# Performance work log

Hardware: AMD Instinct MI355X
Metric: run time of the kernel (lower is better)

Reference implementation:

```python
import jax, jax.numpy as jnp
import numpy as np

N_NODES = 100000
N_EDGES = 1600000
D = 64


def setup_inputs() -> dict:
    key = jax.random.key(0)
    k0, k1, k2, k3 = jax.random.split(key, 4)
    x = jax.random.normal(k0, (N_NODES, D), dtype=jnp.float32)
    edge_index = jax.random.randint(k1, (2, N_EDGES), 0, N_NODES, dtype=jnp.int64)
    W1 = jax.random.normal(k2, (D, D), dtype=jnp.float32) * 0.1
    b1 = jnp.zeros((D,), dtype=jnp.float32)
    W2 = jax.random.normal(k3, (D, D), dtype=jnp.float32) * 0.1
    b2 = jnp.zeros((D,), dtype=jnp.float32)
    return {"x": x, "edge_index": edge_index, "W1": W1, "b1": b1, "W2": W2, "b2": b2}


def _gcn_layer(x, edge_index, W, b):
    n = x.shape[0]
    h = x @ W  # [N, Dout] -- transform before aggregation (small GEMM)
    loop = jnp.arange(n, dtype=edge_index.dtype)
    src = jnp.concatenate([edge_index[0], loop])
    dst = jnp.concatenate([edge_index[1], loop])
    deg = jax.ops.segment_sum(jnp.ones_like(dst, dtype=h.dtype), dst, num_segments=n)
    dinv = jax.lax.rsqrt(deg)  # deg >= 1 thanks to self loops
    norm = dinv[src] * dinv[dst]  # [E+N]
    msg = h[src] * norm[:, None]  # gather: [E+N, Dout]
    agg = jax.ops.segment_sum(msg, dst, num_segments=n)  # scatter-add
    return agg + b


def reference(x, edge_index, W1, b1, W2, b2):
    # dropout p = 0.0 -> identity
    h = jax.nn.relu(_gcn_layer(x, edge_index, W1, b1))
    h = jax.nn.relu(_gcn_layer(h, edge_index, W2, b2))
    return h
```

## Files before the change

### kernel.cpp

```cpp
#include <hip/hip_runtime.h>
#include <hip/hip_bf16.h>

#define D 64
#define NB_HIST 256
#define MAXBK 512

typedef float vfloat4 __attribute__((ext_vector_type(4)));
typedef short short8 __attribute__((ext_vector_type(8)));
typedef float f32x4 __attribute__((ext_vector_type(4)));

__device__ __forceinline__ unsigned short f2bf(float f) {
    union { float f; unsigned u; } v; v.f = f;
    unsigned r = (v.u + 0x7FFF + ((v.u >> 16) & 1)) >> 16;
    return (unsigned short)r;
}
__device__ __forceinline__ unsigned short bftrunc(float f) {
    union { float f; unsigned u; } v; v.f = f;
    return (unsigned short)(v.u >> 16);
}
__device__ __forceinline__ float bffrom(unsigned short h) {
    union { unsigned u; float f; } v; v.u = ((unsigned)h) << 16; return v.f;
}
__device__ __forceinline__ float bflo(unsigned u) {
    union { unsigned u; float f; } v; v.u = u << 16; return v.f;
}
__device__ __forceinline__ float bfhi(unsigned u) {
    union { unsigned u; float f; } v; v.u = u & 0xFFFF0000u; return v.f;
}

__global__ __launch_bounds__(256) void passA_hist_wfrag(
    const int* __restrict__ dst, int* __restrict__ blockCounts, int E, int per, int NBK,
    const float* __restrict__ W1, const float* __restrict__ W2,
    unsigned short* __restrict__ WfH1, unsigned short* __restrict__ WfL1,
    unsigned short* __restrict__ WfH2, unsigned short* __restrict__ WfL2)
{
    int tid = threadIdx.x;

    if ((int)blockIdx.x < NB_HIST) {
        __shared__ int hist[MAXBK];
        for (int i = tid; i < NBK; i += 256) hist[i] = 0;
        __syncthreads();
        int lo = blockIdx.x * per, hi = min(E, lo + per);
        for (int i = lo + tid * 4; i < hi; i += 1024) {
            if (i + 3 < hi) {
                int4 d4 = *(const int4*)(dst + i);
                atomicAdd(&hist[d4.x >> 8], 1);
                atomicAdd(&hist[d4.y >> 8], 1);
                atomicAdd(&hist[d4.z >> 8], 1);
                atomicAdd(&hist[d4.w >> 8], 1);
            } else {
                for (int k = i; k < hi; ++k) atomicAdd(&hist[dst[k] >> 8], 1);
            }
        }
        __syncthreads();
        for (int i = tid; i < NBK; i += 256)
            blockCounts[(size_t)blockIdx.x * NBK + i] = hist[i];
        return;
    }

    int b = (int)blockIdx.x - NB_HIST;
    const float* Wsrc = (b >> 1) ? W2 : W1;
    unsigned short* fh = (b >> 1) ? WfH2 : WfH1;
    unsigned short* fl = (b >> 1) ? WfL2 : WfL1;
    int combo = (b & 1) * 4 + (tid >> 6);
    int lane = tid & 63;
    int s = combo >> 2, c = combo & 3, g = lane >> 4, rl = lane & 15;
#pragma unroll
    for (int j = 0; j < 8; ++j) {
        float v = Wsrc[(32 * s + 8 * g + j) * D + 16 * c + rl];
        unsigned short h = bftrunc(v);
        fh[combo * 512 + lane * 8 + j] = h;
        fl[combo * 512 + lane * 8 + j] = f2bf(v - bffrom(h));
    }
}

__global__ __launch_bounds__(256) void scan_cols(
    const int* __restrict__ blockCounts, int* __restrict__ partial,
    int* __restrict__ totals, int NBK)
{
    int wave = threadIdx.x >> 6, lane = threadIdx.x & 63;
    int k = blockIdx.x * 4 + wave;
    if (k >= NBK) return;
    int carry = 0;
    for (int base = 0; base < NB_HIST; base += 64) {
        int b = base + lane;
        int v = blockCounts[(size_t)b * NBK + k];
        int inc = v;
        for (int d = 1; d < 64; d <<= 1) {
            int t = __shfl_up(inc, d, 64);
            if (lane >= d) inc += t;
        }
        partial[(size_t)k * NB_HIST + b] = inc - v + carry;
        carry += __shfl(inc, 63, 64);
    }
    if (lane == 0) totals[k] = carry;
}

__global__ void scan_buckets(const int* __restrict__ totals, int* __restrict__ bofs, int NBK) {
    int lane = threadIdx.x;
    int carry = 0;
    for (int base = 0; base < NBK; base += 64) {
        int i = base + lane;
        int v = (i < NBK) ? totals[i] : 0;
        int inc = v;
        for (int d = 1; d < 64; d <<= 1) {
            int t = __shfl_up(inc, d, 64);
            if (lane >= d) inc += t;
        }
        if (i < NBK) bofs[i] = inc - v + carry;
        carry += __shfl(inc, 63, 64);
    }
}

__global__ __launch_bounds__(256) void passB(
    const int* __restrict__ src, const int* __restrict__ dst,
    const int* __restrict__ bofs, const int* __restrict__ partial,
    int* __restrict__ bucketed, int E, int per, int NBK)
{
    __shared__ int cur[MAXBK];
    int tid = threadIdx.x, b = blockIdx.x;
    for (int i = tid; i < NBK; i += 256)
        cur[i] = bofs[i] + partial[(size_t)i * NB_HIST + b];
    __syncthreads();
    int lo = b * per, hi = min(E, lo + per);
    for (int i = lo + tid * 4; i < hi; i += 1024) {
        if (i + 3 < hi) {
            int4 d4 = *(const int4*)(dst + i);
            int4 s4 = *(const int4*)(src + i);
            int p0 = atomicAdd(&cur[d4.x >> 8], 1);
            int p1 = atomicAdd(&cur[d4.y >> 8], 1);
            int p2 = atomicAdd(&cur[d4.z >> 8], 1);
            int p3 = atomicAdd(&cur[d4.w >> 8], 1);
            bucketed[p0] = (s4.x << 8) | (d4.x & 255);
            bucketed[p1] = (s4.y << 8) | (d4.y & 255);
            bucketed[p2] = (s4.z << 8) | (d4.z & 255);
            bucketed[p3] = (s4.w << 8) | (d4.w & 255);
        } else {
            for (int k = i; k < hi; ++k) {
                int d = dst[k], s = src[k];
                int pos = atomicAdd(&cur[d >> 8], 1);
                bucketed[pos] = (s << 8) | (d & 255);
            }
        }
    }
}

__global__ __launch_bounds__(256) void build_csr(
    const int* __restrict__ bucketed, const int* __restrict__ bofs,
    const int* __restrict__ totals, int* __restrict__ deg, float* __restrict__ dinv,
    int* __restrict__ ofs, int* __restrict__ csr, int N)
{
    __shared__ int h[256];
    __shared__ int scn[256];
    int tid = threadIdx.x, k = blockIdx.x;
    int e0 = bofs[k], e1 = e0 + totals[k];
    int node = k * 256 + tid;

    h[tid] = 0;
    __syncthreads();
    for (int i = e0 + tid; i < e1; i += 256)
        atomicAdd(&h[bucketed[i] & 255], 1);
    __syncthreads();

    int mydeg = h[tid];
    scn[tid] = mydeg;
    __syncthreads();
    for (int d2 = 1; d2 < 256; d2 <<= 1) {
        int t = (tid >= d2) ? scn[tid - d2] : 0;
        __syncthreads();
        scn[tid] += t;
        __syncthreads();
    }
    int myofs = scn[tid] - mydeg;

    if (node < N) {
        deg[node]  = mydeg;
        dinv[node] = rsqrtf((float)(mydeg + 1));
        ofs[node]  = e0 + myofs;
    }

    h[tid] = myofs;
    __syncthreads();
    for (int i = e0 + tid; i < e1; i += 256) {
        int v = bucketed[i];
        int pos = atomicAdd(&h[v & 255], 1);
        csr[e0 + pos] = v >> 8;
    }
}

__global__ __launch_bounds__(256) void gemm1_mfma(
    const float* __restrict__ X,
    const unsigned short* __restrict__ WfH, const unsigned short* __restrict__ WfL,
    const float* __restrict__ dinv, unsigned short* __restrict__ hn, int N)
{
    int t = threadIdx.x, wave = t >> 6, lane = t & 63;
    int rowBase = (int)blockIdx.x * 64 + wave * 16;
    if (rowBase >= N) return;
    int g = lane >> 4, rl = lane & 15;

    short8 BH[2][4], BL[2][4];
#pragma unroll
    for (int s = 0; s < 2; ++s)
#pragma unroll
        for (int c = 0; c < 4; ++c) {
            BH[s][c] = *(const short8*)(WfH + ((s * 4 + c) * 64 + lane) * 8);
            BL[s][c] = *(const short8*)(WfL + ((s * 4 + c) * 64 + lane) * 8);
        }

    int arow = rowBase + rl; if (arow >= N) arow = N - 1;
    const float* xr = X + (size_t)arow * D;

    f32x4 acc[4];
#pragma unroll
    for (int c = 0; c < 4; ++c) acc[c] = (f32x4){0.f, 0.f, 0.f, 0.f};

#pragma unroll
    for (int s = 0; s < 2; ++s) {
        vfloat4 x0 = *(const vfloat4*)(xr + 32 * s + 8 * g);
        vfloat4 x1 = *(const vfloat4*)(xr + 32 * s + 8 * g + 4);
        short8 ah, al;
#pragma unroll
        for (int j = 0; j < 4; ++j) {
            unsigned short h0 = bftrunc(x0[j]);
            ah[j] = (short)h0; al[j] = (short)f2bf(x0[j] - bffrom(h0));
            unsigned short h1 = bftrunc(x1[j]);
            ah[j + 4] = (short)h1; al[j + 4] = (short)f2bf(x1[j] - bffrom(h1));
        }
#pragma unroll
        for (int c = 0; c < 4; ++c)
            acc[c] = __builtin_amdgcn_mfma_f32_16x16x32_bf16(ah, BH[s][c], acc[c], 0, 0, 0);
#pragma unroll
        for (int c = 0; c < 4; ++c)
            acc[c] = __builtin_amdgcn_mfma_f32_16x16x32_bf16(ah, BL[s][c], acc[c], 0, 0, 0);
#pragma unroll
        for (int c = 0; c < 4; ++c)
            acc[c] = __builtin_amdgcn_mfma_f32_16x16x32_bf16(al, BH[s][c], acc[c], 0, 0, 0);
    }

#pragma unroll
    for (int r = 0; r < 4; ++r) {
        int row = rowBase + g * 4 + r;
        if (row < N) {
            float dv = dinv[row];
            unsigned short* hr = hn + (size_t)row * D + rl;
#pragma unroll
            for (int c = 0; c < 4; ++c) hr[c * 16] = f2bf(acc[c][r] * dv);
        }
    }
}

__global__ __launch_bounds__(256) void agg1_gemm2(
    const int* __restrict__ ofs, const int* __restrict__ deg,
    const int* __restrict__ csr, const unsigned short* __restrict__ hnA,
    const float* __restrict__ dinv, const float* __restrict__ bias,
    const unsigned short* __restrict__ WfH, const unsigned short* __restrict__ WfL,
    unsigned short* __restrict__ hnB, int N)
{
    __shared__ unsigned short sH[32 * 72];
    int tid  = threadIdx.x;
    int lane = tid & 63, wave = tid >> 6;
    int grp  = lane >> 3, sub = lane & 7;
    int rowInBlk = wave * 8 + grp;
    int nodeBase = (int)blockIdx.x * 32;
    int node = nodeBase + rowInBlk;
    bool live = (node < N);

    const int4* hrow = (const int4*)hnA;
    float2 a0 = {0.f, 0.f}, a1 = {0.f, 0.f}, a2 = {0.f, 0.f}, a3 = {0.f, 0.f};

    int s0 = 0, cnt = 0;
    if (live) {
        s0  = ofs[node];
        cnt = deg[node];
        int4 h = hrow[(size_t)node * 8 + sub];
        a0.x += bflo(h.x); a0.y += bfhi(h.x);
        a1.x += bflo(h.y); a1.y += bfhi(h.y);
        a2.x += bflo(h.z); a2.y += bfhi(h.z);
        a3.x += bflo(h.w); a3.y += bfhi(h.w);
    }

    const int* cp = csr + s0;
    int j = 0;
    for (; j + 3 < cnt; j += 4) {
        int sA = cp[j], sB = cp[j + 1], sC = cp[j + 2], sD = cp[j + 3];
        int4 hA = hrow[(size_t)sA * 8 + sub];
        int4 hB = hrow[(size_t)sB * 8 + sub];
        int4 hC = hrow[(size_t)sC * 8 + sub];
        int4 hD = hrow[(size_t)sD * 8 + sub];
        a0.x += bflo(hA.x); a0.y += bfhi(hA.x);
        a1.x += bflo(hA.y); a1.y += bfhi(hA.y);
        a2.x += bflo(hA.z); a2.y += bfhi(hA.z);
        a3.x += bflo(hA.w); a3.y += bfhi(hA.w);
        a0.x += bflo(hB.x); a0.y += bfhi(hB.x);
        a1.x += bflo(hB.y); a1.y += bfhi(hB.y);
        a2.x += bflo(hB.z); a2.y += bfhi(hB.z);
        a3.x += bflo(hB.w); a3.y += bfhi(hB.w);
        a0.x += bflo(hC.x); a0.y += bfhi(hC.x);
        a1.x += bflo(hC.y); a1.y += bfhi(hC.y);
        a2.x += bflo(hC.z); a2.y += bfhi(hC.z);
        a3.x += bflo(hC.w); a3.y += bfhi(hC.w);
        a0.x += bflo(hD.x); a0.y += bfhi(hD.x);
        a1.x += bflo(hD.y); a1.y += bfhi(hD.y);
        a2.x += bflo(hD.z); a2.y += bfhi(hD.z);
        a3.x += bflo(hD.w); a3.y += bfhi(hD.w);
    }
    for (; j < cnt; ++j) {
        int sA = cp[j];
        int4 hA = hrow[(size_t)sA * 8 + sub];
        a0.x += bflo(hA.x); a0.y += bfhi(hA.x);
        a1.x += bflo(hA.y); a1.y += bfhi(hA.y);
        a2.x += bflo(hA.z); a2.y += bfhi(hA.z);
        a3.x += bflo(hA.w); a3.y += bfhi(hA.w);
    }

    {
        float dw = live ? dinv[node] : 0.f;
        float4 b0 = ((const float4*)bias)[sub * 2];
        float4 b1 = ((const float4*)bias)[sub * 2 + 1];
        float o0 = fmaxf(a0.x * dw + b0.x, 0.f);
        float o1 = fmaxf(a0.y * dw + b0.y, 0.f);
        float o2 = fmaxf(a1.x * dw + b0.z, 0.f);
        float o3 = fmaxf(a1.y * dw + b0.w, 0.f);
        float o4 = fmaxf(a2.x * dw + b1.x, 0.f);
        float o5 = fmaxf(a2.y * dw + b1.y, 0.f);
        float o6 = fmaxf(a3.x * dw + b1.z, 0.f);
        float o7 = fmaxf(a3.y * dw + b1.w, 0.f);
        unsigned r0 = (unsigned)f2bf(o0) | ((unsigned)f2bf(o1) << 16);
        unsigned r1 = (unsigned)f2bf(o2) | ((unsigned)f2bf(o3) << 16);
        unsigned r2 = (unsigned)f2bf(o4) | ((unsigned)f2bf(o5) << 16);
        unsigned r3 = (unsigned)f2bf(o6) | ((unsigned)f2bf(o7) << 16);
        *(int4*)&sH[rowInBlk * 72 + sub * 8] = make_int4((int)r0, (int)r1, (int)r2, (int)r3);
    }
    __syncthreads();

    if (wave < 2) {
        int g = lane >> 4, rl = lane & 15;
        f32x4 acc[4];
#pragma unroll
        for (int c = 0; c < 4; ++c) acc[c] = (f32x4){0.f, 0.f, 0.f, 0.f};

#pragma unroll
        for (int s = 0; s < 2; ++s) {
            short8 a = *(const short8*)&sH[(wave * 16 + rl) * 72 + 32 * s + 8 * g];
            short8 BH[4], BL[4];
#pragma unroll
            for (int c = 0; c < 4; ++c) {
                BH[c] = *(const short8*)(WfH + ((s * 4 + c) * 64 + lane) * 8);
                BL[c] = *(const short8*)(WfL + ((s * 4 + c) * 64 + lane) * 8);
            }
#pragma unroll
            for (int c = 0; c < 4; ++c)
                acc[c] = __builtin_amdgcn_mfma_f32_16x16x32_bf16(a, BH[c], acc[c], 0, 0, 0);
#pragma unroll
            for (int c = 0; c < 4; ++c)
                acc[c] = __builtin_amdgcn_mfma_f32_16x16x32_bf16(a, BL[c], acc[c], 0, 0, 0);
        }

#pragma unroll
        for (int r = 0; r < 4; ++r) {
            int row = nodeBase + wave * 16 + g * 4 + r;
            if (row < N) {
                float dv = dinv[row];
                unsigned short* hw = hnB + (size_t)row * D + rl;
#pragma unroll
                for (int c = 0; c < 4; ++c) hw[c * 16] = f2bf(acc[c][r] * dv);
            }
        }
    }
}

template <bool BF16OUT>
__global__ __launch_bounds__(256) void aggregate_relu(
    const int* __restrict__ ofs, const int* __restrict__ deg,
    const int* __restrict__ csr, const unsigned short* __restrict__ hn,
    const float* __restrict__ dinv, const float* __restrict__ bias,
    void* __restrict__ outv, int N)
{
    int t    = blockIdx.x * 256 + threadIdx.x;
    int lane = threadIdx.x & 63;
    int grp  = lane >> 3, sub = lane & 7;
    int node = (t >> 6) * 8 + grp;
    bool live = (node < N);

    const int4* hrow = (const int4*)hn;
    float2 a0 = {0.f, 0.f}, a1 = {0.f, 0.f}, a2 = {0.f, 0.f}, a3 = {0.f, 0.f};

    int s0 = 0, cnt = 0;
    if (live) {
        s0  = ofs[node];
        cnt = deg[node];
        int4 h = hrow[(size_t)node * 8 + sub];
        a0.x += bflo(h.x); a0.y += bfhi(h.x);
        a1.x += bflo(h.y); a1.y += bfhi(h.y);
        a2.x += bflo(h.z); a2.y += bfhi(h.z);
        a3.x += bflo(h.w); a3.y += bfhi(h.w);
    }

    const int* cp = csr + s0;
    int j = 0;
    for (; j + 3 < cnt; j += 4) {
        int sA = cp[j], sB = cp[j + 1], sC = cp[j + 2], sD = cp[j + 3];
        int4 hA = hrow[(size_t)sA * 8 + sub];
        int4 hB = hrow[(size_t)sB * 8 + sub];
        int4 hC = hrow[(size_t)sC * 8 + sub];
        int4 hD = hrow[(size_t)sD * 8 + sub];
        a0.x += bflo(hA.x); a0.y += bfhi(hA.x);
        a1.x += bflo(hA.y); a1.y += bfhi(hA.y);
        a2.x += bflo(hA.z); a2.y += bfhi(hA.z);
        a3.x += bflo(hA.w); a3.y += bfhi(hA.w);
        a0.x += bflo(hB.x); a0.y += bfhi(hB.x);
        a1.x += bflo(hB.y); a1.y += bfhi(hB.y);
        a2.x += bflo(hB.z); a2.y += bfhi(hB.z);
        a3.x += bflo(hB.w); a3.y += bfhi(hB.w);
        a0.x += bflo(hC.x); a0.y += bfhi(hC.x);
        a1.x += bflo(hC.y); a1.y += bfhi(hC.y);
        a2.x += bflo(hC.z); a2.y += bfhi(hC.z);
        a3.x += bflo(hC.w); a3.y += bfhi(hC.w);
        a0.x += bflo(hD.x); a0.y += bfhi(hD.x);
        a1.x += bflo(hD.y); a1.y += bfhi(hD.y);
        a2.x += bflo(hD.z); a2.y += bfhi(hD.z);
        a3.x += bflo(hD.w); a3.y += bfhi(hD.w);
    }
    for (; j < cnt; ++j) {
        int sA = cp[j];
        int4 hA = hrow[(size_t)sA * 8 + sub];
        a0.x += bflo(hA.x); a0.y += bfhi(hA.x);
        a1.x += bflo(hA.y); a1.y += bfhi(hA.y);
        a2.x += bflo(hA.z); a2.y += bfhi(hA.z);
        a3.x += bflo(hA.w); a3.y += bfhi(hA.w);
    }

    if (live) {
        float dw = dinv[node];
        float4 b0 = ((const float4*)bias)[sub * 2];
        float4 b1 = ((const float4*)bias)[sub * 2 + 1];
        float o0 = fmaxf(a0.x * dw + b0.x, 0.f);
        float o1 = fmaxf(a0.y * dw + b0.y, 0.f);
        float o2 = fmaxf(a1.x * dw + b0.z, 0.f);
        float o3 = fmaxf(a1.y * dw + b0.w, 0.f);
        float o4 = fmaxf(a2.x * dw + b1.x, 0.f);
        float o5 = fmaxf(a2.y * dw + b1.y, 0.f);
        float o6 = fmaxf(a3.x * dw + b1.z, 0.f);
        float o7 = fmaxf(a3.y * dw + b1.w, 0.f);
        if (BF16OUT) {
            unsigned r0 = (unsigned)f2bf(o0) | ((unsigned)f2bf(o1) << 16);
            unsigned r1 = (unsigned)f2bf(o2) | ((unsigned)f2bf(o3) << 16);
            unsigned r2 = (unsigned)f2bf(o4) | ((unsigned)f2bf(o5) << 16);
            unsigned r3 = (unsigned)f2bf(o6) | ((unsigned)f2bf(o7) << 16);
            ((int4*)outv)[(size_t)node * 8 + sub] =
                make_int4((int)r0, (int)r1, (int)r2, (int)r3);
        } else {
            float4 v0 = make_float4(o0, o1, o2, o3);
            float4 v1 = make_float4(o4, o5, o6, o7);
            ((float4*)outv)[(size_t)node * 16 + sub * 2]     = v0;
            ((float4*)outv)[(size_t)node * 16 + sub * 2 + 1] = v1;
        }
    }
}


extern "C" void kernel_launch(void* const* d_in, const int* in_sizes, int n_in,
                              void* d_out, int out_size, void* d_ws, size_t ws_size,
                              hipStream_t stream) {
    const float* x   = (const float*)d_in[0];
    const int*   ei  = (const int*)d_in[1];
    const float* W1  = (const float*)d_in[2];
    const float* b1  = (const float*)d_in[3];
    const float* W2  = (const float*)d_in[4];
    const float* b2  = (const float*)d_in[5];

    int N = in_sizes[0] / D;
    int E = in_sizes[1] / 2;
    const int* src = ei;
    const int* dst = ei + E;
    int NBK = (N + 255) >> 8;
    int per = (((E + NB_HIST - 1) / NB_HIST) + 3) & ~3;

    char* ws = (char*)d_ws;
    int*            blockCounts = (int*)(ws + 0x00000000);
    int*            partial     = (int*)(ws + 0x00080000);
    int*            totals      = (int*)(ws + 0x00100000);
    int*            bofs        = (int*)(ws + 0x00110000);
    int*            deg         = (int*)(ws + 0x00120000);
    float*          dinv        = (float*)(ws + 0x00190000);
    int*            ofs         = (int*)(ws + 0x00200000);
    int*            bucketed    = (int*)(ws + 0x00280000);
    int*            csr         = (int*)(ws + 0x00A00000);
    unsigned short* hnA         = (unsigned short*)(ws + 0x01100000);
    unsigned short* hnB         = (unsigned short*)(ws + 0x01D80000);
    unsigned short* WfH1        = (unsigned short*)(ws + 0x02A80000);
    unsigned short* WfL1        = WfH1 + 4096;
    unsigned short* WfH2        = WfL1 + 4096;
    unsigned short* WfL2        = WfH2 + 4096;
    float*          outF        = (float*)d_out;

    int nb_G = (N + 63) / 64;
    int nb_A = (N + 31) / 32;

    passA_hist_wfrag<<<NB_HIST + 4, 256, 0, stream>>>(dst, blockCounts, E, per, NBK,
                                                      W1, W2, WfH1, WfL1, WfH2, WfL2);
    scan_cols<<<(NBK + 3) / 4, 256, 0, stream>>>(blockCounts, partial, totals, NBK);
    scan_buckets<<<1, 64, 0, stream>>>(totals, bofs, NBK);
    passB<<<NB_HIST, 256, 0, stream>>>(src, dst, bofs, partial, bucketed, E, per, NBK);
    build_csr<<<NBK, 256, 0, stream>>>(bucketed, bofs, totals, deg, dinv, ofs, csr, N);

    gemm1_mfma<<<nb_G, 256, 0, stream>>>(x, WfH1, WfL1, dinv, hnA, N);
    agg1_gemm2<<<nb_A, 256, 0, stream>>>(ofs, deg, csr, hnA, dinv, b1, WfH2, WfL2, hnB, N);
    aggregate_relu<false><<<nb_A, 256, 0, stream>>>(ofs, deg, csr, hnB, dinv, b2, (void*)outF, N);
}
```

Baseline: 204.3 us.

## Build CSR with direct global-atomic counting sort instead of bucketed two-pass sort

Replaces the multi-kernel bucket sort (per-block LDS histograms over 256-node buckets, column scans, bucket scatter, then per-bucket CSR build) with a flat counting sort. It counts per-node degrees with global atomics, scans the degrees in two small kernels, then scatters each source into the CSR with returning global atomics on per-node cursors. The aim is fewer launches and less intermediate traffic, since the bucketed array is no longer written and re-read. The cost is heavy global atomic traffic with returned values, a nondeterministic neighbor order within each node, and a scan that assumes at most 64 scan blocks.

```diff
diff --git a/kernel.cpp b/kernel.cpp
--- a/kernel.cpp
+++ b/kernel.cpp
@@ -2,8 +2,7 @@
 #include <hip/hip_bf16.h>
 
 #define D 64
-#define NB_HIST 256
-#define MAXBK 512
+#define NB_CNT 1024
 
 typedef float vfloat4 __attribute__((ext_vector_type(4)));
 typedef short short8 __attribute__((ext_vector_type(8)));
@@ -28,37 +27,31 @@
     union { unsigned u; float f; } v; v.u = u & 0xFFFF0000u; return v.f;
 }
 
-__global__ __launch_bounds__(256) void passA_hist_wfrag(
-    const int* __restrict__ dst, int* __restrict__ blockCounts, int E, int per, int NBK,
+__global__ __launch_bounds__(256) void count_wfrag(
+    const int* __restrict__ dst, int E, int* __restrict__ deg,
     const float* __restrict__ W1, const float* __restrict__ W2,
     unsigned short* __restrict__ WfH1, unsigned short* __restrict__ WfL1,
     unsigned short* __restrict__ WfH2, unsigned short* __restrict__ WfL2)
 {
     int tid = threadIdx.x;
 
-    if ((int)blockIdx.x < NB_HIST) {
-        __shared__ int hist[MAXBK];
-        for (int i = tid; i < NBK; i += 256) hist[i] = 0;
-        __syncthreads();
-        int lo = blockIdx.x * per, hi = min(E, lo + per);
-        for (int i = lo + tid * 4; i < hi; i += 1024) {
-            if (i + 3 < hi) {
+    if ((int)blockIdx.x < NB_CNT) {
+        int stride = NB_CNT * 1024;
+        for (int i = ((int)blockIdx.x * 256 + tid) * 4; i < E; i += stride) {
+            if (i + 3 < E) {
                 int4 d4 = *(const int4*)(dst + i);
-                atomicAdd(&hist[d4.x >> 8], 1);
-                atomicAdd(&hist[d4.y >> 8], 1);
-                atomicAdd(&hist[d4.z >> 8], 1);
-                atomicAdd(&hist[d4.w >> 8], 1);
+                atomicAdd(&deg[d4.x], 1);
+                atomicAdd(&deg[d4.y], 1);
+                atomicAdd(&deg[d4.z], 1);
+                atomicAdd(&deg[d4.w], 1);
             } else {
-                for (int k = i; k < hi; ++k) atomicAdd(&hist[dst[k] >> 8], 1);
+                for (int k = i; k < E; ++k) atomicAdd(&deg[dst[k]], 1);
             }
         }
-        __syncthreads();
-        for (int i = tid; i < NBK; i += 256)
-            blockCounts[(size_t)blockIdx.x * NBK + i] = hist[i];
         return;
     }
 
-    int b = (int)blockIdx.x - NB_HIST;
+    int b = (int)blockIdx.x - NB_CNT;
     const float* Wsrc = (b >> 1) ? W2 : W1;
     unsigned short* fh = (b >> 1) ? WfH2 : WfH1;
     unsigned short* fl = (b >> 1) ? WfL2 : WfL1;
@@ -74,117 +67,91 @@
     }
 }
 
-__global__ __launch_bounds__(256) void scan_cols(
-    const int* __restrict__ blockCounts, int* __restrict__ partial,
-    int* __restrict__ totals, int NBK)
-{
-    int wave = threadIdx.x >> 6, lane = threadIdx.x & 63;
-    int k = blockIdx.x * 4 + wave;
-    if (k >= NBK) return;
-    int carry = 0;
-    for (int base = 0; base < NB_HIST; base += 64) {
-        int b = base + lane;
-        int v = blockCounts[(size_t)b * NBK + k];
+__global__ __launch_bounds__(256) void scan_sums(
+    const int* __restrict__ deg, int* __restrict__ bsum, int N)
+{
+    __shared__ int wsum[4];
+    int tid = threadIdx.x, lane = tid & 63, wave = tid >> 6;
+    int base = (int)blockIdx.x * 2048 + tid * 8;
+    int s = 0;
+#pragma unroll
+    for (int k = 0; k < 8; ++k) {
+        int i = base + k;
+        if (i < N) s += deg[i];
+    }
+    for (int d = 32; d >= 1; d >>= 1) s += __shfl_xor(s, d, 64);
+    if (lane == 0) wsum[wave] = s;
+    __syncthreads();
+    if (tid == 0) bsum[blockIdx.x] = wsum[0] + wsum[1] + wsum[2] + wsum[3];
+}
+
+__global__ __launch_bounds__(256) void scan_write(
+    const int* __restrict__ deg, const int* __restrict__ bsum,
+    int* __restrict__ ofs, int* __restrict__ cur, float* __restrict__ dinv,
+    int N, int SB)
+{
+    __shared__ int sBase;
+    __shared__ int wsum[4];
+    int tid = threadIdx.x, lane = tid & 63, wave = tid >> 6;
+
+    if (wave == 0) {
+        int v = (lane < SB) ? bsum[lane] : 0;
         int inc = v;
         for (int d = 1; d < 64; d <<= 1) {
             int t = __shfl_up(inc, d, 64);
             if (lane >= d) inc += t;
         }
-        partial[(size_t)k * NB_HIST + b] = inc - v + carry;
-        carry += __shfl(inc, 63, 64);
-    }
-    if (lane == 0) totals[k] = carry;
-}
-
-__global__ void scan_buckets(const int* __restrict__ totals, int* __restrict__ bofs, int NBK) {
-    int lane = threadIdx.x;
-    int carry = 0;
-    for (int base = 0; base < NBK; base += 64) {
-        int i = base + lane;
-        int v = (i < NBK) ? totals[i] : 0;
-        int inc = v;
-        for (int d = 1; d < 64; d <<= 1) {
-            int t = __shfl_up(inc, d, 64);
-            if (lane >= d) inc += t;
-        }
-        if (i < NBK) bofs[i] = inc - v + carry;
-        carry += __shfl(inc, 63, 64);
-    }
-}
-
-__global__ __launch_bounds__(256) void passB(
+        if (lane == (int)blockIdx.x) sBase = inc - v;
+    }
+
+    int base = (int)blockIdx.x * 2048 + tid * 8;
+    int v[8], p[8], t8 = 0;
+#pragma unroll
+    for (int k = 0; k < 8; ++k) {
+        int i = base + k;
+        v[k] = (i < N) ? deg[i] : 0;
+        p[k] = t8;
+        t8 += v[k];
+    }
+    int inc = t8;
+    for (int d = 1; d < 64; d <<= 1) {
+        int t = __shfl_up(inc, d, 64);
+        if (lane >= d) inc += t;
+    }
+    if (lane == 63) wsum[wave] = inc;
+    __syncthreads();
+
+    int wbase = 0;
+    for (int w = 0; w < wave; ++w) wbase += wsum[w];
+    int ebase = sBase + wbase + inc - t8;
+#pragma unroll
+    for (int k = 0; k < 8; ++k) {
+        int i = base + k;
+        if (i < N) {
+            int o = ebase + p[k];
+            ofs[i] = o;
+            cur[i] = o;
+            dinv[i] = rsqrtf((float)v[k] + 1.0f);
+        }
+    }
+}
+
+__global__ __launch_bounds__(256) void scatter_csr(
     const int* __restrict__ src, const int* __restrict__ dst,
-    const int* __restrict__ bofs, const int* __restrict__ partial,
-    int* __restrict__ bucketed, int E, int per, int NBK)
-{
-    __shared__ int cur[MAXBK];
-    int tid = threadIdx.x, b = blockIdx.x;
-    for (int i = tid; i < NBK; i += 256)
-        cur[i] = bofs[i] + partial[(size_t)i * NB_HIST + b];
-    __syncthreads();
-    int lo = b * per, hi = min(E, lo + per);
-    for (int i = lo + tid * 4; i < hi; i += 1024) {
-        if (i + 3 < hi) {
+    int* __restrict__ cur, int* __restrict__ csr, int E)
+{
+    int stride = NB_CNT * 1024;
+    for (int i = ((int)blockIdx.x * 256 + threadIdx.x) * 4; i < E; i += stride) {
+        if (i + 3 < E) {
             int4 d4 = *(const int4*)(dst + i);
             int4 s4 = *(const int4*)(src + i);
-            int p0 = atomicAdd(&cur[d4.x >> 8], 1);
-            int p1 = atomicAdd(&cur[d4.y >> 8], 1);
-            int p2 = atomicAdd(&cur[d4.z >> 8], 1);
-            int p3 = atomicAdd(&cur[d4.w >> 8], 1);
-            bucketed[p0] = (s4.x << 8) | (d4.x & 255);
-            bucketed[p1] = (s4.y << 8) | (d4.y & 255);
-            bucketed[p2] = (s4.z << 8) | (d4.z & 255);
-            bucketed[p3] = (s4.w << 8) | (d4.w & 255);
+            csr[atomicAdd(&cur[d4.x], 1)] = s4.x;
+            csr[atomicAdd(&cur[d4.y], 1)] = s4.y;
+            csr[atomicAdd(&cur[d4.z], 1)] = s4.z;
+            csr[atomicAdd(&cur[d4.w], 1)] = s4.w;
         } else {
-            for (int k = i; k < hi; ++k) {
-                int d = dst[k], s = src[k];
-                int pos = atomicAdd(&cur[d >> 8], 1);
-                bucketed[pos] = (s << 8) | (d & 255);
-            }
-        }
-    }
-}
-
-__global__ __launch_bounds__(256) void build_csr(
-    const int* __restrict__ bucketed, const int* __restrict__ bofs,
-    const int* __restrict__ totals, int* __restrict__ deg, float* __restrict__ dinv,
-    int* __restrict__ ofs, int* __restrict__ csr, int N)
-{
-    __shared__ int h[256];
-    __shared__ int scn[256];
-    int tid = threadIdx.x, k = blockIdx.x;
-    int e0 = bofs[k], e1 = e0 + totals[k];
-    int node = k * 256 + tid;
-
-    h[tid] = 0;
-    __syncthreads();
-    for (int i = e0 + tid; i < e1; i += 256)
-        atomicAdd(&h[bucketed[i] & 255], 1);
-    __syncthreads();
-
-    int mydeg = h[tid];
-    scn[tid] = mydeg;
-    __syncthreads();
-    for (int d2 = 1; d2 < 256; d2 <<= 1) {
-        int t = (tid >= d2) ? scn[tid - d2] : 0;
-        __syncthreads();
-        scn[tid] += t;
-        __syncthreads();
-    }
-    int myofs = scn[tid] - mydeg;
-
-    if (node < N) {
-        deg[node]  = mydeg;
-        dinv[node] = rsqrtf((float)(mydeg + 1));
-        ofs[node]  = e0 + myofs;
-    }
-
-    h[tid] = myofs;
-    __syncthreads();
-    for (int i = e0 + tid; i < e1; i += 256) {
-        int v = bucketed[i];
-        int pos = atomicAdd(&h[v & 255], 1);
-        csr[e0 + pos] = v >> 8;
+            for (int k = i; k < E; ++k) csr[atomicAdd(&cur[dst[k]], 1)] = src[k];
+        }
     }
 }
 
@@ -369,12 +336,11 @@
     }
 }
 
-template <bool BF16OUT>
-__global__ __launch_bounds__(256) void aggregate_relu(
+__global__ __launch_bounds__(256) void aggregate_relu_f32(
     const int* __restrict__ ofs, const int* __restrict__ deg,
     const int* __restrict__ csr, const unsigned short* __restrict__ hn,
     const float* __restrict__ dinv, const float* __restrict__ bias,
-    void* __restrict__ outv, int N)
+    float* __restrict__ outF, int N)
 {
     int t    = blockIdx.x * 256 + threadIdx.x;
     int lane = threadIdx.x & 63;
@@ -442,19 +408,10 @@
         float o5 = fmaxf(a2.y * dw + b1.y, 0.f);
         float o6 = fmaxf(a3.x * dw + b1.z, 0.f);
         float o7 = fmaxf(a3.y * dw + b1.w, 0.f);
-        if (BF16OUT) {
-            unsigned r0 = (unsigned)f2bf(o0) | ((unsigned)f2bf(o1) << 16);
-            unsigned r1 = (unsigned)f2bf(o2) | ((unsigned)f2bf(o3) << 16);
-            unsigned r2 = (unsigned)f2bf(o4) | ((unsigned)f2bf(o5) << 16);
-            unsigned r3 = (unsigned)f2bf(o6) | ((unsigned)f2bf(o7) << 16);
-            ((int4*)outv)[(size_t)node * 8 + sub] =
-                make_int4((int)r0, (int)r1, (int)r2, (int)r3);
-        } else {
-            float4 v0 = make_float4(o0, o1, o2, o3);
-            float4 v1 = make_float4(o4, o5, o6, o7);
-            ((float4*)outv)[(size_t)node * 16 + sub * 2]     = v0;
-            ((float4*)outv)[(size_t)node * 16 + sub * 2 + 1] = v1;
-        }
+        float4 v0 = make_float4(o0, o1, o2, o3);
+        float4 v1 = make_float4(o4, o5, o6, o7);
+        ((float4*)outF)[(size_t)node * 16 + sub * 2]     = v0;
+        ((float4*)outF)[(size_t)node * 16 + sub * 2 + 1] = v1;
     }
 }
 
@@ -473,38 +430,33 @@
     int E = in_sizes[1] / 2;
     const int* src = ei;
     const int* dst = ei + E;
-    int NBK = (N + 255) >> 8;
-    int per = (((E + NB_HIST - 1) / NB_HIST) + 3) & ~3;
+    int SB = (N + 2047) / 2048;
 
     char* ws = (char*)d_ws;
-    int*            blockCounts = (int*)(ws + 0x00000000);
-    int*            partial     = (int*)(ws + 0x00080000);
-    int*            totals      = (int*)(ws + 0x00100000);
-    int*            bofs        = (int*)(ws + 0x00110000);
-    int*            deg         = (int*)(ws + 0x00120000);
-    float*          dinv        = (float*)(ws + 0x00190000);
-    int*            ofs         = (int*)(ws + 0x00200000);
-    int*            bucketed    = (int*)(ws + 0x00280000);
-    int*            csr         = (int*)(ws + 0x00A00000);
-    unsigned short* hnA         = (unsigned short*)(ws + 0x01100000);
-    unsigned short* hnB         = (unsigned short*)(ws + 0x01D80000);
-    unsigned short* WfH1        = (unsigned short*)(ws + 0x02A80000);
-    unsigned short* WfL1        = WfH1 + 4096;
-    unsigned short* WfH2        = WfL1 + 4096;
-    unsigned short* WfL2        = WfH2 + 4096;
-    float*          outF        = (float*)d_out;
+    int*            deg  = (int*)(ws + 0x00000000);
+    float*          dinv = (float*)(ws + 0x00080000);
+    int*            ofs  = (int*)(ws + 0x00100000);
+    int*            cur  = (int*)(ws + 0x00180000);
+    int*            bsum = (int*)(ws + 0x00200000);
+    int*            csr  = (int*)(ws + 0x00210000);
+    unsigned short* hnA  = (unsigned short*)(ws + 0x00A40000);
+    unsigned short* hnB  = (unsigned short*)(ws + 0x01700000);
+    unsigned short* WfH1 = (unsigned short*)(ws + 0x023C0000);
+    unsigned short* WfL1 = WfH1 + 4096;
+    unsigned short* WfH2 = WfL1 + 4096;
+    unsigned short* WfL2 = WfH2 + 4096;
+    float*          outF = (float*)d_out;
 
     int nb_G = (N + 63) / 64;
     int nb_A = (N + 31) / 32;
 
-    passA_hist_wfrag<<<NB_HIST + 4, 256, 0, stream>>>(dst, blockCounts, E, per, NBK,
-                                                      W1, W2, WfH1, WfL1, WfH2, WfL2);
-    scan_cols<<<(NBK + 3) / 4, 256, 0, stream>>>(blockCounts, partial, totals, NBK);
-    scan_buckets<<<1, 64, 0, stream>>>(totals, bofs, NBK);
-    passB<<<NB_HIST, 256, 0, stream>>>(src, dst, bofs, partial, bucketed, E, per, NBK);
-    build_csr<<<NBK, 256, 0, stream>>>(bucketed, bofs, totals, deg, dinv, ofs, csr, N);
+    hipMemsetAsync(deg, 0, (size_t)N * 4, stream);
+    count_wfrag<<<NB_CNT + 4, 256, 0, stream>>>(dst, E, deg, W1, W2, WfH1, WfL1, WfH2, WfL2);
+    scan_sums<<<SB, 256, 0, stream>>>(deg, bsum, N);
+    scan_write<<<SB, 256, 0, stream>>>(deg, bsum, ofs, cur, dinv, N, SB);
+    scatter_csr<<<NB_CNT, 256, 0, stream>>>(src, dst, cur, csr, E);
 
     gemm1_mfma<<<nb_G, 256, 0, stream>>>(x, WfH1, WfL1, dinv, hnA, N);
     agg1_gemm2<<<nb_A, 256, 0, stream>>>(ofs, deg, csr, hnA, dinv, b1, WfH2, WfL2, hnB, N);
-    aggregate_relu<false><<<nb_A, 256, 0, stream>>>(ofs, deg, csr, hnB, dinv, b2, (void*)outF, N);
-}
+    aggregate_relu_f32<<<nb_A, 256, 0, stream>>>(ofs, deg, csr, hnB, dinv, b2, outF, N);
+}
```

Result: slower. 347.7 us (+70.2%).

## Bin CSR neighbors by source range to improve gather locality

Applied to the files above, without the earlier changes.

The CSR build now sub-sorts each node's neighbor list into 8 bins by source index range and stores per-bin counts packed as bytes. Both aggregation kernels walk the bins in order, so the lanes of a wave tend to gather rows from the same source region at about the same time, aiming for better cache hit rates. In exchange the inner loops become shorter per bin, which reduces the effect of the 4-way unroll, and build_csr does more shared-memory atomics and setup. A bin count above 255 would overflow its byte field.

```diff
diff --git a/kernel.cpp b/kernel.cpp
--- a/kernel.cpp
+++ b/kernel.cpp
@@ -4,6 +4,7 @@
 #define D 64
 #define NB_HIST 256
 #define MAXBK 512
+#define QSHIFT 14
 
 typedef float vfloat4 __attribute__((ext_vector_type(4)));
 typedef short short8 __attribute__((ext_vector_type(8)));
@@ -148,21 +149,25 @@
 __global__ __launch_bounds__(256) void build_csr(
     const int* __restrict__ bucketed, const int* __restrict__ bofs,
     const int* __restrict__ totals, int* __restrict__ deg, float* __restrict__ dinv,
-    int* __restrict__ ofs, int* __restrict__ csr, int N)
-{
-    __shared__ int h[256];
+    int* __restrict__ ofs, int2* __restrict__ qcnt, int* __restrict__ csr, int N)
+{
+    __shared__ int h8[256 * 8];
     __shared__ int scn[256];
     int tid = threadIdx.x, k = blockIdx.x;
     int e0 = bofs[k], e1 = e0 + totals[k];
     int node = k * 256 + tid;
 
-    h[tid] = 0;
-    __syncthreads();
-    for (int i = e0 + tid; i < e1; i += 256)
-        atomicAdd(&h[bucketed[i] & 255], 1);
-    __syncthreads();
-
-    int mydeg = h[tid];
+    for (int i = tid; i < 2048; i += 256) h8[i] = 0;
+    __syncthreads();
+    for (int i = e0 + tid; i < e1; i += 256) {
+        int v = bucketed[i];
+        atomicAdd(&h8[(v & 255) * 8 + ((v >> 8) >> QSHIFT)], 1);
+    }
+    __syncthreads();
+
+    int c[8]; int mydeg = 0;
+#pragma unroll
+    for (int b = 0; b < 8; ++b) { c[b] = h8[tid * 8 + b]; mydeg += c[b]; }
     scn[tid] = mydeg;
     __syncthreads();
     for (int d2 = 1; d2 < 256; d2 <<= 1) {
@@ -177,14 +182,20 @@
         deg[node]  = mydeg;
         dinv[node] = rsqrtf((float)(mydeg + 1));
         ofs[node]  = e0 + myofs;
-    }
-
-    h[tid] = myofs;
+        int lo = c[0] | (c[1] << 8) | (c[2] << 16) | (c[3] << 24);
+        int hi = c[4] | (c[5] << 8) | (c[6] << 16) | (c[7] << 24);
+        qcnt[node] = make_int2(lo, hi);
+    }
+
+    int run = myofs;
+#pragma unroll
+    for (int b = 0; b < 8; ++b) { h8[tid * 8 + b] = run; run += c[b]; }
     __syncthreads();
     for (int i = e0 + tid; i < e1; i += 256) {
         int v = bucketed[i];
-        int pos = atomicAdd(&h[v & 255], 1);
-        csr[e0 + pos] = v >> 8;
+        int s = v >> 8;
+        int pos = atomicAdd(&h8[(v & 255) * 8 + (s >> QSHIFT)], 1);
+        csr[e0 + pos] = s;
     }
 }
 
@@ -249,8 +260,36 @@
     }
 }
 
+#define ACC1(h)                                   \
+    a0.x += bflo((h).x); a0.y += bfhi((h).x);     \
+    a1.x += bflo((h).y); a1.y += bfhi((h).y);     \
+    a2.x += bflo((h).z); a2.y += bfhi((h).z);     \
+    a3.x += bflo((h).w); a3.y += bfhi((h).w);
+
+#define BIN_GATHER_LOOP                                                   \
+    for (int bb = 0; bb < 8; ++bb) {                                      \
+        int cnt = (int)(qlo & 255u);                                      \
+        qlo = (qlo >> 8) | (qhi << 24);                                   \
+        qhi >>= 8;                                                        \
+        int j = 0;                                                        \
+        for (; j + 3 < cnt; j += 4) {                                     \
+            int sA = cp[j], sB = cp[j + 1], sC = cp[j + 2], sD = cp[j + 3]; \
+            int4 hA = hrow[(size_t)sA * 8 + sub];                         \
+            int4 hB = hrow[(size_t)sB * 8 + sub];                         \
+            int4 hC = hrow[(size_t)sC * 8 + sub];                         \
+            int4 hD = hrow[(size_t)sD * 8 + sub];                         \
+            ACC1(hA); ACC1(hB); ACC1(hC); ACC1(hD);                       \
+        }                                                                 \
+        for (; j < cnt; ++j) {                                            \
+            int sA = cp[j];                                               \
+            int4 hA = hrow[(size_t)sA * 8 + sub];                         \
+            ACC1(hA);                                                     \
+        }                                                                 \
+        cp += cnt;                                                        \
+    }
+
 __global__ __launch_bounds__(256) void agg1_gemm2(
-    const int* __restrict__ ofs, const int* __restrict__ deg,
+    const int* __restrict__ ofs, const int2* __restrict__ qcnt,
     const int* __restrict__ csr, const unsigned short* __restrict__ hnA,
     const float* __restrict__ dinv, const float* __restrict__ bias,
     const unsigned short* __restrict__ WfH, const unsigned short* __restrict__ WfL,
@@ -268,50 +307,18 @@
     const int4* hrow = (const int4*)hnA;
     float2 a0 = {0.f, 0.f}, a1 = {0.f, 0.f}, a2 = {0.f, 0.f}, a3 = {0.f, 0.f};
 
-    int s0 = 0, cnt = 0;
+    int s0 = 0;
+    unsigned qlo = 0, qhi = 0;
     if (live) {
-        s0  = ofs[node];
-        cnt = deg[node];
+        s0 = ofs[node];
+        int2 qc = qcnt[node];
+        qlo = (unsigned)qc.x; qhi = (unsigned)qc.y;
         int4 h = hrow[(size_t)node * 8 + sub];
-        a0.x += bflo(h.x); a0.y += bfhi(h.x);
-        a1.x += bflo(h.y); a1.y += bfhi(h.y);
-        a2.x += bflo(h.z); a2.y += bfhi(h.z);
-        a3.x += bflo(h.w); a3.y += bfhi(h.w);
+        ACC1(h);
     }
 
     const int* cp = csr + s0;
-    int j = 0;
-    for (; j + 3 < cnt; j += 4) {
-        int sA = cp[j], sB = cp[j + 1], sC = cp[j + 2], sD = cp[j + 3];
-        int4 hA = hrow[(size_t)sA * 8 + sub];
-        int4 hB = hrow[(size_t)sB * 8 + sub];
-        int4 hC = hrow[(size_t)sC * 8 + sub];
-        int4 hD = hrow[(size_t)sD * 8 + sub];
-        a0.x += bflo(hA.x); a0.y += bfhi(hA.x);
-        a1.x += bflo(hA.y); a1.y += bfhi(hA.y);
-        a2.x += bflo(hA.z); a2.y += bfhi(hA.z);
-        a3.x += bflo(hA.w); a3.y += bfhi(hA.w);
-        a0.x += bflo(hB.x); a0.y += bfhi(hB.x);
-        a1.x += bflo(hB.y); a1.y += bfhi(hB.y);
-        a2.x += bflo(hB.z); a2.y += bfhi(hB.z);
-        a3.x += bflo(hB.w); a3.y += bfhi(hB.w);
-        a0.x += bflo(hC.x); a0.y += bfhi(hC.x);
-        a1.x += bflo(hC.y); a1.y += bfhi(hC.y);
-        a2.x += bflo(hC.z); a2.y += bfhi(hC.z);
-        a3.x += bflo(hC.w); a3.y += bfhi(hC.w);
-        a0.x += bflo(hD.x); a0.y += bfhi(hD.x);
-        a1.x += bflo(hD.y); a1.y += bfhi(hD.y);
-        a2.x += bflo(hD.z); a2.y += bfhi(hD.z);
-        a3.x += bflo(hD.w); a3.y += bfhi(hD.w);
-    }
-    for (; j < cnt; ++j) {
-        int sA = cp[j];
-        int4 hA = hrow[(size_t)sA * 8 + sub];
-        a0.x += bflo(hA.x); a0.y += bfhi(hA.x);
-        a1.x += bflo(hA.y); a1.y += bfhi(hA.y);
-        a2.x += bflo(hA.z); a2.y += bfhi(hA.z);
-        a3.x += bflo(hA.w); a3.y += bfhi(hA.w);
-    }
+    BIN_GATHER_LOOP;
 
     {
         float dw = live ? dinv[node] : 0.f;
@@ -369,12 +376,11 @@
     }
 }
 
-template <bool BF16OUT>
-__global__ __launch_bounds__(256) void aggregate_relu(
-    const int* __restrict__ ofs, const int* __restrict__ deg,
+__global__ __launch_bounds__(256) void aggregate_relu_f32(
+    const int* __restrict__ ofs, const int2* __restrict__ qcnt,
     const int* __restrict__ csr, const unsigned short* __restrict__ hn,
     const float* __restrict__ dinv, const float* __restrict__ bias,
-    void* __restrict__ outv, int N)
+    float* __restrict__ outF, int N)
 {
     int t    = blockIdx.x * 256 + threadIdx.x;
     int lane = threadIdx.x & 63;
@@ -385,50 +391,18 @@
     const int4* hrow = (const int4*)hn;
     float2 a0 = {0.f, 0.f}, a1 = {0.f, 0.f}, a2 = {0.f, 0.f}, a3 = {0.f, 0.f};
 
-    int s0 = 0, cnt = 0;
+    int s0 = 0;
+    unsigned qlo = 0, qhi = 0;
     if (live) {
-        s0  = ofs[node];
-        cnt = deg[node];
+        s0 = ofs[node];
+        int2 qc = qcnt[node];
+        qlo = (unsigned)qc.x; qhi = (unsigned)qc.y;
         int4 h = hrow[(size_t)node * 8 + sub];
-        a0.x += bflo(h.x); a0.y += bfhi(h.x);
-        a1.x += bflo(h.y); a1.y += bfhi(h.y);
-        a2.x += bflo(h.z); a2.y += bfhi(h.z);
-        a3.x += bflo(h.w); a3.y += bfhi(h.w);
+        ACC1(h);
     }
 
     const int* cp = csr + s0;
-    int j = 0;
-    for (; j + 3 < cnt; j += 4) {
-        int sA = cp[j], sB = cp[j + 1], sC = cp[j + 2], sD = cp[j + 3];
-        int4 hA = hrow[(size_t)sA * 8 + sub];
-        int4 hB = hrow[(size_t)sB * 8 + sub];
-        int4 hC = hrow[(size_t)sC * 8 + sub];
-        int4 hD = hrow[(size_t)sD * 8 + sub];
-        a0.x += bflo(hA.x); a0.y += bfhi(hA.x);
-        a1.x += bflo(hA.y); a1.y += bfhi(hA.y);
-        a2.x += bflo(hA.z); a2.y += bfhi(hA.z);
-        a3.x += bflo(hA.w); a3.y += bfhi(hA.w);
-        a0.x += bflo(hB.x); a0.y += bfhi(hB.x);
-        a1.x += bflo(hB.y); a1.y += bfhi(hB.y);
-        a2.x += bflo(hB.z); a2.y += bfhi(hB.z);
-        a3.x += bflo(hB.w); a3.y += bfhi(hB.w);
-        a0.x += bflo(hC.x); a0.y += bfhi(hC.x);
-        a1.x += bflo(hC.y); a1.y += bfhi(hC.y);
-        a2.x += bflo(hC.z); a2.y += bfhi(hC.z);
-        a3.x += bflo(hC.w); a3.y += bfhi(hC.w);
-        a0.x += bflo(hD.x); a0.y += bfhi(hD.x);
-        a1.x += bflo(hD.y); a1.y += bfhi(hD.y);
-        a2.x += bflo(hD.z); a2.y += bfhi(hD.z);
-        a3.x += bflo(hD.w); a3.y += bfhi(hD.w);
-    }
-    for (; j < cnt; ++j) {
-        int sA = cp[j];
-        int4 hA = hrow[(size_t)sA * 8 + sub];
-        a0.x += bflo(hA.x); a0.y += bfhi(hA.x);
-        a1.x += bflo(hA.y); a1.y += bfhi(hA.y);
-        a2.x += bflo(hA.z); a2.y += bfhi(hA.z);
-        a3.x += bflo(hA.w); a3.y += bfhi(hA.w);
-    }
+    BIN_GATHER_LOOP;
 
     if (live) {
         float dw = dinv[node];
@@ -442,19 +416,10 @@
         float o5 = fmaxf(a2.y * dw + b1.y, 0.f);
         float o6 = fmaxf(a3.x * dw + b1.z, 0.f);
         float o7 = fmaxf(a3.y * dw + b1.w, 0.f);
-        if (BF16OUT) {
-            unsigned r0 = (unsigned)f2bf(o0) | ((unsigned)f2bf(o1) << 16);
-            unsigned r1 = (unsigned)f2bf(o2) | ((unsigned)f2bf(o3) << 16);
-            unsigned r2 = (unsigned)f2bf(o4) | ((unsigned)f2bf(o5) << 16);
-            unsigned r3 = (unsigned)f2bf(o6) | ((unsigned)f2bf(o7) << 16);
-            ((int4*)outv)[(size_t)node * 8 + sub] =
-                make_int4((int)r0, (int)r1, (int)r2, (int)r3);
-        } else {
-            float4 v0 = make_float4(o0, o1, o2, o3);
-            float4 v1 = make_float4(o4, o5, o6, o7);
-            ((float4*)outv)[(size_t)node * 16 + sub * 2]     = v0;
-            ((float4*)outv)[(size_t)node * 16 + sub * 2 + 1] = v1;
-        }
+        float4 v0 = make_float4(o0, o1, o2, o3);
+        float4 v1 = make_float4(o4, o5, o6, o7);
+        ((float4*)outF)[(size_t)node * 16 + sub * 2]     = v0;
+        ((float4*)outF)[(size_t)node * 16 + sub * 2 + 1] = v1;
     }
 }
 
@@ -479,6 +444,7 @@
     char* ws = (char*)d_ws;
     int*            blockCounts = (int*)(ws + 0x00000000);
     int*            partial     = (int*)(ws + 0x00080000);
+    int2*           qcnt        = (int2*)(ws + 0x00000000);
     int*            totals      = (int*)(ws + 0x00100000);
     int*            bofs        = (int*)(ws + 0x00110000);
     int*            deg         = (int*)(ws + 0x00120000);
@@ -502,9 +468,9 @@
     scan_cols<<<(NBK + 3) / 4, 256, 0, stream>>>(blockCounts, partial, totals, NBK);
     scan_buckets<<<1, 64, 0, stream>>>(totals, bofs, NBK);
     passB<<<NB_HIST, 256, 0, stream>>>(src, dst, bofs, partial, bucketed, E, per, NBK);
-    build_csr<<<NBK, 256, 0, stream>>>(bucketed, bofs, totals, deg, dinv, ofs, csr, N);
+    build_csr<<<NBK, 256, 0, stream>>>(bucketed, bofs, totals, deg, dinv, ofs, qcnt, csr, N);
 
     gemm1_mfma<<<nb_G, 256, 0, stream>>>(x, WfH1, WfL1, dinv, hnA, N);
-    agg1_gemm2<<<nb_A, 256, 0, stream>>>(ofs, deg, csr, hnA, dinv, b1, WfH2, WfL2, hnB, N);
-    aggregate_relu<false><<<nb_A, 256, 0, stream>>>(ofs, deg, csr, hnB, dinv, b2, (void*)outF, N);
-}
+    agg1_gemm2<<<nb_A, 256, 0, stream>>>(ofs, qcnt, csr, hnA, dinv, b1, WfH2, WfL2, hnB, N);
+    aggregate_relu_f32<<<nb_A, 256, 0, stream>>>(ofs, qcnt, csr, hnB, dinv, b2, outF, N);
+}
```

After: 234.2 us. 1.15x slower.

## Fold bucket scan into passB/build_csr and coarsely sort CSR neighbors by source

Applied to the files above, without the earlier changes.

Removes the single-block scan_buckets launch by having each passB block recompute the bucket prefix scan in shared memory, and each build_csr block compute its own edge offset with a wave reduction over totals. build_csr now counts per (destination, source-range) sub-bin, using 8 bins per node keyed on the high bits of src, so each node's neighbor list comes out roughly sorted by source. This is meant to improve gather locality in the aggregation kernels and to cut one launch, at the cost of redundant scans, 8x larger shared histograms and more shared-memory atomics.

```diff
diff --git a/kernel.cpp b/kernel.cpp
--- a/kernel.cpp
+++ b/kernel.cpp
@@ -4,6 +4,7 @@
 #define D 64
 #define NB_HIST 256
 #define MAXBK 512
+#define QSHIFT 14
 
 typedef float vfloat4 __attribute__((ext_vector_type(4)));
 typedef short short8 __attribute__((ext_vector_type(8)));
@@ -96,32 +97,34 @@
     if (lane == 0) totals[k] = carry;
 }
 
-__global__ void scan_buckets(const int* __restrict__ totals, int* __restrict__ bofs, int NBK) {
-    int lane = threadIdx.x;
-    int carry = 0;
-    for (int base = 0; base < NBK; base += 64) {
-        int i = base + lane;
-        int v = (i < NBK) ? totals[i] : 0;
-        int inc = v;
-        for (int d = 1; d < 64; d <<= 1) {
-            int t = __shfl_up(inc, d, 64);
-            if (lane >= d) inc += t;
-        }
-        if (i < NBK) bofs[i] = inc - v + carry;
-        carry += __shfl(inc, 63, 64);
-    }
-}
-
 __global__ __launch_bounds__(256) void passB(
     const int* __restrict__ src, const int* __restrict__ dst,
-    const int* __restrict__ bofs, const int* __restrict__ partial,
+    const int* __restrict__ totals, const int* __restrict__ partial,
     int* __restrict__ bucketed, int E, int per, int NBK)
 {
     __shared__ int cur[MAXBK];
+    __shared__ int sBofs[MAXBK];
     int tid = threadIdx.x, b = blockIdx.x;
+
+    if (tid < 64) {
+        int carry = 0;
+        for (int base = 0; base < NBK; base += 64) {
+            int i = base + tid;
+            int v = (i < NBK) ? totals[i] : 0;
+            int inc = v;
+            for (int d = 1; d < 64; d <<= 1) {
+                int t = __shfl_up(inc, d, 64);
+                if (tid >= d) inc += t;
+            }
+            if (i < NBK) sBofs[i] = inc - v + carry;
+            carry += __shfl(inc, 63, 64);
+        }
+    }
+    __syncthreads();
     for (int i = tid; i < NBK; i += 256)
-        cur[i] = bofs[i] + partial[(size_t)i * NB_HIST + b];
-    __syncthreads();
+        cur[i] = sBofs[i] + partial[(size_t)i * NB_HIST + b];
+    __syncthreads();
+
     int lo = b * per, hi = min(E, lo + per);
     for (int i = lo + tid * 4; i < hi; i += 1024) {
         if (i + 3 < hi) {
@@ -146,23 +149,36 @@
 }
 
 __global__ __launch_bounds__(256) void build_csr(
-    const int* __restrict__ bucketed, const int* __restrict__ bofs,
-    const int* __restrict__ totals, int* __restrict__ deg, float* __restrict__ dinv,
+    const int* __restrict__ bucketed, const int* __restrict__ totals,
+    int* __restrict__ deg, float* __restrict__ dinv,
     int* __restrict__ ofs, int* __restrict__ csr, int N)
 {
-    __shared__ int h[256];
+    __shared__ int h8[256 * 8];
     __shared__ int scn[256];
+    __shared__ int sE0;
     int tid = threadIdx.x, k = blockIdx.x;
-    int e0 = bofs[k], e1 = e0 + totals[k];
+
+    if (tid < 64) {
+        int s = 0;
+        for (int i = tid; i < k; i += 64) s += totals[i];
+        for (int d = 32; d >= 1; d >>= 1) s += __shfl_xor(s, d, 64);
+        if (tid == 0) sE0 = s;
+    }
+    for (int i = tid; i < 2048; i += 256) h8[i] = 0;
+    __syncthreads();
+
+    int e0 = sE0, e1 = e0 + totals[k];
     int node = k * 256 + tid;
 
-    h[tid] = 0;
-    __syncthreads();
-    for (int i = e0 + tid; i < e1; i += 256)
-        atomicAdd(&h[bucketed[i] & 255], 1);
-    __syncthreads();
-
-    int mydeg = h[tid];
+    for (int i = e0 + tid; i < e1; i += 256) {
+        int v = bucketed[i];
+        atomicAdd(&h8[((v & 255) << 3) | ((unsigned)(v >> 8) >> QSHIFT)], 1);
+    }
+    __syncthreads();
+
+    int c[8]; int mydeg = 0;
+#pragma unroll
+    for (int b = 0; b < 8; ++b) { c[b] = h8[tid * 8 + b]; mydeg += c[b]; }
     scn[tid] = mydeg;
     __syncthreads();
     for (int d2 = 1; d2 < 256; d2 <<= 1) {
@@ -179,12 +195,15 @@
         ofs[node]  = e0 + myofs;
     }
 
-    h[tid] = myofs;
+    int run = myofs;
+#pragma unroll
+    for (int b = 0; b < 8; ++b) { h8[tid * 8 + b] = run; run += c[b]; }
     __syncthreads();
     for (int i = e0 + tid; i < e1; i += 256) {
         int v = bucketed[i];
-        int pos = atomicAdd(&h[v & 255], 1);
-        csr[e0 + pos] = v >> 8;
+        int s = v >> 8;
+        int pos = atomicAdd(&h8[((v & 255) << 3) | ((unsigned)s >> QSHIFT)], 1);
+        csr[e0 + pos] = s;
     }
 }
 
@@ -369,12 +388,11 @@
     }
 }
 
-template <bool BF16OUT>
-__global__ __launch_bounds__(256) void aggregate_relu(
+__global__ __launch_bounds__(256) void aggregate_relu_f32(
     const int* __restrict__ ofs, const int* __restrict__ deg,
     const int* __restrict__ csr, const unsigned short* __restrict__ hn,
     const float* __restrict__ dinv, const float* __restrict__ bias,
-    void* __restrict__ outv, int N)
+    float* __restrict__ outF, int N)
 {
     int t    = blockIdx.x * 256 + threadIdx.x;
     int lane = threadIdx.x & 63;
@@ -442,19 +460,10 @@
         float o5 = fmaxf(a2.y * dw + b1.y, 0.f);
         float o6 = fmaxf(a3.x * dw + b1.z, 0.f);
         float o7 = fmaxf(a3.y * dw + b1.w, 0.f);
-        if (BF16OUT) {
-            unsigned r0 = (unsigned)f2bf(o0) | ((unsigned)f2bf(o1) << 16);
-            unsigned r1 = (unsigned)f2bf(o2) | ((unsigned)f2bf(o3) << 16);
-            unsigned r2 = (unsigned)f2bf(o4) | ((unsigned)f2bf(o5) << 16);
-            unsigned r3 = (unsigned)f2bf(o6) | ((unsigned)f2bf(o7) << 16);
-            ((int4*)outv)[(size_t)node * 8 + sub] =
-                make_int4((int)r0, (int)r1, (int)r2, (int)r3);
-        } else {
-            float4 v0 = make_float4(o0, o1, o2, o3);
-            float4 v1 = make_float4(o4, o5, o6, o7);
-            ((float4*)outv)[(size_t)node * 16 + sub * 2]     = v0;
-            ((float4*)outv)[(size_t)node * 16 + sub * 2 + 1] = v1;
-        }
+        float4 v0 = make_float4(o0, o1, o2, o3);
+        float4 v1 = make_float4(o4, o5, o6, o7);
+        ((float4*)outF)[(size_t)node * 16 + sub * 2]     = v0;
+        ((float4*)outF)[(size_t)node * 16 + sub * 2 + 1] = v1;
     }
 }
 
@@ -480,7 +489,6 @@
     int*            blockCounts = (int*)(ws + 0x00000000);
     int*            partial     = (int*)(ws + 0x00080000);
     int*            totals      = (int*)(ws + 0x00100000);
-    int*            bofs        = (int*)(ws + 0x00110000);
     int*            deg         = (int*)(ws + 0x00120000);
     float*          dinv        = (float*)(ws + 0x00190000);
     int*            ofs         = (int*)(ws + 0x00200000);
@@ -500,11 +508,10 @@
     passA_hist_wfrag<<<NB_HIST + 4, 256, 0, stream>>>(dst, blockCounts, E, per, NBK,
                                                       W1, W2, WfH1, WfL1, WfH2, WfL2);
     scan_cols<<<(NBK + 3) / 4, 256, 0, stream>>>(blockCounts, partial, totals, NBK);
-    scan_buckets<<<1, 64, 0, stream>>>(totals, bofs, NBK);
-    passB<<<NB_HIST, 256, 0, stream>>>(src, dst, bofs, partial, bucketed, E, per, NBK);
-    build_csr<<<NBK, 256, 0, stream>>>(bucketed, bofs, totals, deg, dinv, ofs, csr, N);
+    passB<<<NB_HIST, 256, 0, stream>>>(src, dst, totals, partial, bucketed, E, per, NBK);
+    build_csr<<<NBK, 256, 0, stream>>>(bucketed, totals, deg, dinv, ofs, csr, N);
 
     gemm1_mfma<<<nb_G, 256, 0, stream>>>(x, WfH1, WfL1, dinv, hnA, N);
     agg1_gemm2<<<nb_A, 256, 0, stream>>>(ofs, deg, csr, hnA, dinv, b1, WfH2, WfL2, hnB, N);
-    aggregate_relu<false><<<nb_A, 256, 0, stream>>>(ofs, deg, csr, hnB, dinv, b2, (void*)outF, N);
-}
+    aggregate_relu_f32<<<nb_A, 256, 0, stream>>>(ofs, deg, csr, hnB, dinv, b2, outF, N);
+}
```

New measurement: 199.0 us. 2.6% less time.
